# Optimization experiments

Measured on AMD Instinct MI355X. Metric: run time of the kernel, lower is better.

## Reference

```python
import jax, jax.numpy as jnp
import numpy as np

B, L, D = 2, 2048, 1536
H = 12            # num_heads == num_key_value_heads
FDIM = 16         # feature_dim (per-head q/k dim)
HD = D // H       # head_dim = 128 (per-head v dim)
EPS = 1e-12
W_STD = 0.02


def setup_inputs() -> dict:
    key = jax.random.key(0)
    k0, k1, k2, k3, k4 = jax.random.split(key, 5)
    hidden_states = jax.random.normal(k0, (B, L, D), dtype=jnp.float32)
    Wq = jax.random.normal(k1, (D, H * FDIM), dtype=jnp.float32) * W_STD
    Wk = jax.random.normal(k2, (D, H * FDIM), dtype=jnp.float32) * W_STD
    Wv = jax.random.normal(k3, (D, H * HD), dtype=jnp.float32) * W_STD
    Wo = jax.random.normal(k4, (H * HD, D), dtype=jnp.float32) * W_STD
    return {"hidden_states": hidden_states, "Wq": Wq, "Wk": Wk, "Wv": Wv, "Wo": Wo}


def _split_heads(x, h):
    b, l, hd = x.shape
    return x.reshape(b, l, h, hd // h).transpose(0, 2, 1, 3)  # b h l d


def reference(hidden_states, Wq, Wk, Wv, Wo):
    b, l, _ = hidden_states.shape
    q = _split_heads(hidden_states @ Wq, H)  # [b,h,l,FDIM]
    k = _split_heads(hidden_states @ Wk, H)  # [b,h,l,FDIM]
    v = _split_heads(hidden_states @ Wv, H)  # [b,h,l,HD]

    # parallel_based(q, k, v, eps, use_scale=True, use_normalize=True)
    q = q * (FDIM ** -0.5)
    s = jnp.einsum('bhld,bhmd->bhlm', q, k)            # raw qk scores
    attn = 1.0 + s + 0.5 * s * s                        # 2nd-order Taylor of exp
    causal = jnp.tril(jnp.ones((l, l), dtype=bool))
    attn = jnp.where(causal, attn, 0.0)
    o = jnp.einsum('bhlm,bhmd->bhld', attn, v)          # [b,h,l,HD]
    z = attn.sum(axis=-1)                               # causal normalizer [b,h,l]
    o = o / (z[..., None] + EPS)

    o = o.transpose(0, 2, 1, 3).reshape(b, l, H * HD)   # b l (h d)
    return o @ Wo
```

## Files before the change

kernel.cpp:

```cpp
#include <hip/hip_runtime.h>
#include <hip/hip_bf16.h>

typedef short short8 __attribute__((ext_vector_type(8)));
typedef float f32x4  __attribute__((ext_vector_type(4)));
typedef float f32x16 __attribute__((ext_vector_type(16)));
typedef unsigned int u32x4 __attribute__((ext_vector_type(4)));

union V16   { u32x4 v; short8 s; };
union U16x8 { u32x4 v; unsigned short u[8]; };
union FB4   { u32x4 v; float f[4]; };
union BF2U  { __hip_bfloat162 h; unsigned int u; };

__device__ inline unsigned short f2bf(float f) {
  union { float f; unsigned int u; } x; x.f = f;
  unsigned int u = x.u + 0x7fffu + ((x.u >> 16) & 1u);
  return (unsigned short)(u >> 16);
}

__device__ __forceinline__ unsigned int pkbf(float a, float b) {
  BF2U p; p.h = __float22bfloat162_rn(make_float2(a, b)); return p.u;
}

__device__ __forceinline__ void plswap(unsigned int& a, unsigned int& b) {
  asm("v_permlane32_swap_b32 %0, %1" : "+v"(a), "+v"(b));
}

__device__ __forceinline__ int probe_fp32(const unsigned short* hs) {
  int bad = 0;
#pragma unroll
  for (int i = 0; i < 64; ++i) {
    unsigned int e = (hs[2 * i] >> 7) & 0xFFu;
    if (e >= 0xFEu || (e > 0u && e < 0x60u)) bad++;
  }
  return bad >= 6;
}

__device__ __forceinline__ void gl_lds16(const unsigned short* g, unsigned short* l) {
  __builtin_amdgcn_global_load_lds(
      (const __attribute__((address_space(1))) unsigned int*)g,
      (__attribute__((address_space(3))) unsigned int*)l, 16, 0, 0);
}

__global__ __launch_bounds__(256) void w_tr(const void* __restrict__ Wq,
                                            const void* __restrict__ Wk,
                                            const void* __restrict__ Wv,
                                            const void* __restrict__ Wo,
                                            const void* __restrict__ hs,
                                            unsigned short* __restrict__ WT,
                                            unsigned short* __restrict__ WoT,
                                            unsigned short* __restrict__ hsb) {
  __shared__ unsigned short t[32][33];
  __shared__ int sf;
  if (threadIdx.x == 0) sf = probe_fp32((const unsigned short*)hs);
  __syncthreads();
  const int f = sf;
  const int z = blockIdx.z;
  if (z == 4) {
    size_t i0 = ((size_t)(blockIdx.y * 48 + blockIdx.x) * 256 + threadIdx.x) * 8;
    if (f) {
      const float* in = (const float*)hs;
      FB4 a, b; a.v = *(const u32x4*)&in[i0]; b.v = *(const u32x4*)&in[i0 + 4];
      U16x8 p;
#pragma unroll
      for (int j = 0; j < 4; ++j) { p.u[j] = f2bf(a.f[j]); p.u[j + 4] = f2bf(b.f[j]); }
      *(u32x4*)&hsb[i0] = p.v;
    } else {
      *(u32x4*)&hsb[i0] = *(const u32x4*)((const unsigned short*)hs + i0);
    }
    return;
  }
  if (blockIdx.y >= 48) return;
  const void* in_; unsigned short* out; int C;
  if      (z == 0) { in_ = Wq; out = WT;              C = 192;  }
  else if (z == 1) { in_ = Wk; out = WT + 192 * 1536; C = 192;  }
  else if (z == 2) { in_ = Wv; out = WT + 384 * 1536; C = 1536; }
  else             { in_ = Wo; out = WoT;             C = 1536; }
  const int c0 = blockIdx.x * 32;
  if (c0 >= C) return;
  const int tx = threadIdx.x & 31, ty = threadIdx.x >> 5;
  const int r0 = blockIdx.y * 32;
#pragma unroll
  for (int i = 0; i < 4; ++i) {
    size_t idx = (size_t)(r0 + ty + 8 * i) * C + (c0 + tx);
    t[ty + 8 * i][tx] = f ? f2bf(((const float*)in_)[idx])
                          : ((const unsigned short*)in_)[idx];
  }
  __syncthreads();
#pragma unroll
  for (int i = 0; i < 4; ++i)
    out[(size_t)(c0 + ty + 8 * i) * 1536 + (r0 + tx)] = t[tx][ty + 8 * i];
}

__global__ __launch_bounds__(256) void tr_v(const unsigned short* __restrict__ in_,
                                            unsigned short* __restrict__ out,
                                            int R, int C, int ldin,
                                            long long in_bstride, long long out_bstride) {
  __shared__ unsigned short t[32][33];
  const size_t ibase = (size_t)blockIdx.z * in_bstride;
  const size_t obase = (size_t)blockIdx.z * out_bstride;
  const int tx = threadIdx.x & 31, ty = threadIdx.x >> 5;
  const int r0 = blockIdx.y * 32, c0 = blockIdx.x * 32;
#pragma unroll
  for (int i = 0; i < 4; ++i)
    t[ty + 8 * i][tx] = in_[ibase + (size_t)(r0 + ty + 8 * i) * ldin + (c0 + tx)];
  __syncthreads();
#pragma unroll
  for (int i = 0; i < 4; ++i)
    out[obase + (size_t)(c0 + ty + 8 * i) * R + (r0 + tx)] = t[tx][ty + 8 * i];
}

__global__ __launch_bounds__(256) void gemm_bt(const unsigned short* __restrict__ A,
                                               const unsigned short* __restrict__ BT,
                                               void* __restrict__ C_,
                                               int M, int N, int K,
                                               const unsigned short* __restrict__ probe_src) {
  __shared__ unsigned short As[2][128][64];
  __shared__ unsigned short Bs[2][128][64];
  const int m0 = blockIdx.y * 128, n0 = blockIdx.x * 128;
  const int tid = threadIdx.x;
  const int lane = tid & 63, w = tid >> 6;
  const int wr = w >> 1, wc = w & 1;
  const int quad = lane >> 4, mrow = lane & 15;

  const int sr = lane >> 3;
  const int sc = ((lane & 7) ^ (lane >> 3)) * 8;
  const int fsw = (mrow & 7);

  const f32x4 zf = {0.f, 0.f, 0.f, 0.f};
  f32x4 acc[4][4];
#pragma unroll
  for (int mt = 0; mt < 4; ++mt)
#pragma unroll
    for (int nt = 0; nt < 4; ++nt) acc[mt][nt] = zf;

  const int nk = K >> 6;
#pragma unroll
  for (int j = 0; j < 4; ++j) {
    const int r = 32 * w + 8 * j + sr;
    gl_lds16(&A [(size_t)(m0 + r) * K + sc], &As[0][32 * w + 8 * j][0]);
    gl_lds16(&BT[(size_t)(n0 + r) * K + sc], &Bs[0][32 * w + 8 * j][0]);
  }

  for (int ks = 0; ks < nk; ++ks) {
    const int cur = ks & 1;
    __syncthreads();
    if (ks + 1 < nk) {
      const int k1 = (ks + 1) << 6;
#pragma unroll
      for (int j = 0; j < 4; ++j) {
        const int r = 32 * w + 8 * j + sr;
        gl_lds16(&A [(size_t)(m0 + r) * K + k1 + sc], &As[cur ^ 1][32 * w + 8 * j][0]);
        gl_lds16(&BT[(size_t)(n0 + r) * K + k1 + sc], &Bs[cur ^ 1][32 * w + 8 * j][0]);
      }
    }
#pragma unroll
    for (int kq = 0; kq < 2; ++kq) {
      short8 afr[4], bfr[4];
#pragma unroll
      for (int mt = 0; mt < 4; ++mt) {
        V16 u; u.v = *(const u32x4*)&As[cur][wr * 64 + mt * 16 + mrow][((kq * 4 + quad) ^ fsw) * 8];
        afr[mt] = u.s;
      }
#pragma unroll
      for (int nt = 0; nt < 4; ++nt) {
        V16 u; u.v = *(const u32x4*)&Bs[cur][wc * 64 + nt * 16 + mrow][((kq * 4 + quad) ^ fsw) * 8];
        bfr[nt] = u.s;
      }
#pragma unroll
      for (int mt = 0; mt < 4; ++mt)
#pragma unroll
        for (int nt = 0; nt < 4; ++nt)
          acc[mt][nt] = __builtin_amdgcn_mfma_f32_16x16x32_bf16(afr[mt], bfr[nt], acc[mt][nt], 0, 0, 0);
    }
  }

  const int of = probe_src ? probe_fp32(probe_src) : 0;
#pragma unroll
  for (int mt = 0; mt < 4; ++mt)
#pragma unroll
    for (int nt = 0; nt < 4; ++nt)
#pragma unroll
      for (int r = 0; r < 4; ++r) {
        int grow = m0 + wr * 64 + mt * 16 + quad * 4 + r;
        int gcol = n0 + wc * 64 + nt * 16 + mrow;
        size_t idx = (size_t)grow * N + gcol;
        if (of) ((float*)C_)[idx] = acc[mt][nt][r];
        else    ((unsigned short*)C_)[idx] = f2bf(acc[mt][nt][r]);
      }
}

__global__ __launch_bounds__(256, 3) void attn_based(const unsigned short* __restrict__ qkv,
                                                     const unsigned short* __restrict__ vT,
                                                     unsigned short* __restrict__ obuf) {
  __shared__ unsigned short Vs[2][128][64];
  __shared__ float zbuf[2][32];
  const int LD = 1920;
  const int bh = blockIdx.x;
  const int qt = 31 - blockIdx.y;
  const int b = bh / 12, h = bh % 12;
  const int tid = threadIdx.x;
  const int lane = tid & 63, w = tid >> 6;
  const int qsub = w & 1, kvp = w >> 1;
  const int col = lane & 31, hi = lane >> 5;

  const int q0 = qt * 64 + qsub * 32;
  const int q_abs = q0 + col;

  V16 bq; bq.v = *(const u32x4*)&qkv[(size_t)(b * 2048 + q_abs) * LD + h * 16 + hi * 8];

  const unsigned short* kptr =
      &qkv[(size_t)(b * 2048 + kvp * 32 + col) * LD + 192 + h * 16 + hi * 8];

  const unsigned short* vbase = vT + (size_t)(bh * 128) * 2048;

  const f32x16 z16 = {0.f,0.f,0.f,0.f,0.f,0.f,0.f,0.f,0.f,0.f,0.f,0.f,0.f,0.f,0.f,0.f};
  f32x16 oacc[4];
#pragma unroll
  for (int nc = 0; nc < 4; ++nc) oacc[nc] = z16;
  float zcA[4] = {0.f, 0.f, 0.f, 0.f};

#define STAGE_V(KV0, BUF)                                                     \
  {                                                                           \
    _Pragma("unroll")                                                         \
    for (int j = 0; j < 4; ++j) {                                             \
      const int row = 32 * w + 8 * j + (lane >> 3);                           \
      gl_lds16(vbase + (size_t)row * 2048 + (KV0) + ((lane & 7) ^ (lane >> 3)) * 8, \
               &Vs[BUF][32 * w + 8 * j][0]);                                  \
    }                                                                         \
  }

  STAGE_V(0, 0);
  V16 kf; kf.v = *(const u32x4*)kptr;
  __syncthreads();

  for (int t = 0; t <= qt; ++t) {
    const int cur = t & 1;
    if (t < qt) STAGE_V((t + 1) * 64, cur ^ 1);

    V16 kfn;
    kptr += (size_t)64 * LD;
    if (t < qt) kfn.v = *(const u32x4*)kptr;

    const bool live = (t < qt) | (kvp <= qsub);
    if (live) {
      f32x16 st = __builtin_amdgcn_mfma_f32_32x32x16_bf16(kf.s, bq.s, z16, 0, 0, 0);
      const int kv0 = t * 64 + kvp * 32;
      const bool diag = (t == qt) & (kvp == qsub);
      float pr[16];
      if (diag) {
#pragma unroll
        for (int r = 0; r < 16; ++r) {
          float s = st[r];
          float a = fmaf(s, fmaf(s, 0.03125f, 0.25f), 1.0f);
          const int kvr = kv0 + (r & 3) + 8 * (r >> 2) + 4 * hi;
          a = (kvr <= q_abs) ? a : 0.0f;
          zcA[r & 3] += a; pr[r] = a;
        }
      } else {
#pragma unroll
        for (int r = 0; r < 16; ++r) {
          float s = st[r];
          float a = fmaf(s, fmaf(s, 0.03125f, 0.25f), 1.0f);
          zcA[r & 3] += a; pr[r] = a;
        }
      }

      union PA { short8 s; unsigned int wd[4]; } pa0, pa1;
      {
        unsigned int x0 = pkbf(pr[0], pr[1]), x1 = pkbf(pr[2], pr[3]);
        unsigned int y0 = pkbf(pr[4], pr[5]), y1 = pkbf(pr[6], pr[7]);
        plswap(x0, y0); plswap(x1, y1);
        pa0.wd[0] = x0; pa0.wd[1] = x1; pa0.wd[2] = y0; pa0.wd[3] = y1;
      }
      {
        unsigned int x0 = pkbf(pr[8], pr[9]),  x1 = pkbf(pr[10], pr[11]);
        unsigned int y0 = pkbf(pr[12], pr[13]), y1 = pkbf(pr[14], pr[15]);
        plswap(x0, y0); plswap(x1, y1);
        pa1.wd[0] = x0; pa1.wd[1] = x1; pa1.wd[2] = y0; pa1.wd[3] = y1;
      }

      __builtin_amdgcn_s_setprio(1);
#pragma unroll
      for (int nc = 0; nc < 4; ++nc) {
        const int hd = nc * 32 + col;
        V16 v0, v1;
        v0.v = *(const u32x4*)&Vs[cur][hd][(((kvp * 4 + hi)     ^ (hd & 7)) * 8)];
        v1.v = *(const u32x4*)&Vs[cur][hd][(((kvp * 4 + 2 + hi) ^ (hd & 7)) * 8)];
        oacc[nc] = __builtin_amdgcn_mfma_f32_32x32x16_bf16(pa0.s, v0.s, oacc[nc], 0, 0, 0);
        oacc[nc] = __builtin_amdgcn_mfma_f32_32x32x16_bf16(pa1.s, v1.s, oacc[nc], 0, 0, 0);
      }
      __builtin_amdgcn_s_setprio(0);
    }
    __syncthreads();
    if (t < qt) kf = kfn;
  }

  float zcol = (zcA[0] + zcA[1]) + (zcA[2] + zcA[3]);
  zcol += __shfl_xor(zcol, 32, 64);

  float* fbuf = (float*)&Vs[0][0][0];
  if (w >= 2) {
    const int base = (w & 1) * 4096;
#pragma unroll
    for (int nc = 0; nc < 4; ++nc)
#pragma unroll
      for (int g = 0; g < 4; ++g) {
        f32x4 v = {oacc[nc][4 * g], oacc[nc][4 * g + 1],
                   oacc[nc][4 * g + 2], oacc[nc][4 * g + 3]};
        *(f32x4*)&fbuf[base + ((nc * 4 + g) * 64 + lane) * 4] = v;
      }
    if (lane < 32) zbuf[w & 1][lane] = zcol;
  }
  __syncthreads();
  if (w < 2) {
    const int base = w * 4096;
#pragma unroll
    for (int nc = 0; nc < 4; ++nc)
#pragma unroll
      for (int g = 0; g < 4; ++g) {
        f32x4 v = *(const f32x4*)&fbuf[base + ((nc * 4 + g) * 64 + lane) * 4];
#pragma unroll
        for (int r = 0; r < 4; ++r) oacc[nc][4 * g + r] += v[r];
      }
    const float zinv = 1.0f / (zcol + zbuf[w][col] + 1e-12f);
#pragma unroll
    for (int g = 0; g < 4; ++g)
#pragma unroll
      for (int rr = 0; rr < 4; ++rr) {
        const int qrow = rr + 8 * g + 4 * hi;
        const float iv = __shfl(zinv, qrow, 64);
        const size_t base_o = (size_t)(b * 2048 + q0 + qrow) * 1536 + h * 128 + col;
#pragma unroll
        for (int nc = 0; nc < 4; ++nc)
          obuf[base_o + nc * 32] = f2bf(oacc[nc][4 * g + rr] * iv);
      }
  }
#undef STAGE_V
}

extern "C" void kernel_launch(void* const* d_in, const int* in_sizes, int n_in,
                              void* d_out, int out_size, void* d_ws, size_t ws_size,
                              hipStream_t stream) {
  const void* hs = d_in[0];
  const void* Wq = d_in[1];
  const void* Wk = d_in[2];
  const void* Wv = d_in[3];
  const void* Wo = d_in[4];
  const unsigned short* hsp = (const unsigned short*)hs;

  unsigned short* ws   = (unsigned short*)d_ws;
  unsigned short* WT   = ws;
  unsigned short* WoT  = WT + 1920 * 1536;
  unsigned short* qkvb = WoT + 1536 * 1536;
  unsigned short* hsb  = qkvb + 4096 * 1920;
  unsigned short* vT   = hsb + 4096 * 1536;
  unsigned short* obuf = hsb;

  w_tr<<<dim3(48, 64, 5), 256, 0, stream>>>(Wq, Wk, Wv, Wo, hs, WT, WoT, hsb);

  gemm_bt<<<dim3(15, 32, 1), 256, 0, stream>>>(hsb, WT, qkvb, 4096, 1920, 1536, nullptr);

  tr_v<<<dim3(48, 64, 2), 256, 0, stream>>>(qkvb + 384, vT, 2048, 1536, 1920,
                                            (long long)2048 * 1920, (long long)1536 * 2048);

  attn_based<<<dim3(24, 32, 1), 256, 0, stream>>>(qkvb, vT, obuf);

  gemm_bt<<<dim3(12, 32, 1), 256, 0, stream>>>(obuf, WoT, d_out, 4096, 1536, 1536, hsp);
}
```

Measured before the change: 223.2 us.

## Replace GEMM with 8-wave 256x128 tile, triple-buffered, interleaved MFMA schedule

Swaps the 4-wave 128x128 double-buffered GEMM for an 8-wave kernel with 256x128 tiles and a three-stage LDS ring. Global-to-LDS loads are issued two steps ahead and split across four compute phases. Barriers, sched_barrier pins and setprio bracket each group of MFMAs so the waves stay in lockstep and load issue overlaps matrix math. The aim is to hide global load latency and LDS read stalls in both projection GEMMs. The cost is more LDS per block, more barriers and hand-tuned vmcnt waits that are fragile.

```diff
diff --git a/kernel.cpp b/kernel.cpp
--- a/kernel.cpp
+++ b/kernel.cpp
@@ -40,6 +40,8 @@
       (const __attribute__((address_space(1))) unsigned int*)g,
       (__attribute__((address_space(3))) unsigned int*)l, 16, 0, 0);
 }
+
+#define PIN() __builtin_amdgcn_sched_barrier(0)
 
 __global__ __launch_bounds__(256) void w_tr(const void* __restrict__ Wq,
                                             const void* __restrict__ Wk,
@@ -109,22 +111,31 @@
     out[obase + (size_t)(c0 + ty + 8 * i) * R + (r0 + tx)] = t[tx][ty + 8 * i];
 }
 
-__global__ __launch_bounds__(256) void gemm_bt(const unsigned short* __restrict__ A,
-                                               const unsigned short* __restrict__ BT,
-                                               void* __restrict__ C_,
-                                               int M, int N, int K,
-                                               const unsigned short* __restrict__ probe_src) {
-  __shared__ unsigned short As[2][128][64];
-  __shared__ unsigned short Bs[2][128][64];
-  const int m0 = blockIdx.y * 128, n0 = blockIdx.x * 128;
+__global__ __launch_bounds__(512, 2) void gemm8(const unsigned short* __restrict__ A,
+                                                const unsigned short* __restrict__ BT,
+                                                void* __restrict__ C_,
+                                                int M, int N, int K,
+                                                const unsigned short* __restrict__ probe_src) {
+  __shared__ unsigned short As[3][256][64];
+  __shared__ unsigned short Bs[3][128][64];
+  const int m0 = blockIdx.y * 256, n0 = blockIdx.x * 128;
   const int tid = threadIdx.x;
   const int lane = tid & 63, w = tid >> 6;
   const int wr = w >> 1, wc = w & 1;
   const int quad = lane >> 4, mrow = lane & 15;
+  const int fsw = (mrow & 7);
 
   const int sr = lane >> 3;
-  const int sc = ((lane & 7) ^ (lane >> 3)) * 8;
-  const int fsw = (mrow & 7);
+  const int sc = ((lane & 7) ^ sr) * 8;
+  const unsigned short* Ab = A  + (size_t)(m0 + 32 * w + sr) * K + sc;
+  const unsigned short* Bb = BT + (size_t)(n0 + 16 * w + sr) * K + sc;
+
+#define STAGE_A(T2, J) gl_lds16(Ab + (size_t)(8 * (J)) * K + (size_t)(T2) * 64, \
+                                &As[(T2) % 3][32 * w + 8 * (J)][0])
+#define STAGE_B(T2, J) gl_lds16(Bb + (size_t)(8 * (J)) * K + (size_t)(T2) * 64, \
+                                &Bs[(T2) % 3][16 * w + 8 * (J)][0])
+#define RD_A(dst, mt, kq) { V16 u_; u_.v = *(const u32x4*)&As[cur][wr * 64 + (mt) * 16 + mrow][(((kq) * 4 + quad) ^ fsw) * 8]; dst = u_.s; }
+#define RD_B(dst, nt, kq) { V16 u_; u_.v = *(const u32x4*)&Bs[cur][wc * 64 + (nt) * 16 + mrow][(((kq) * 4 + quad) ^ fsw) * 8]; dst = u_.s; }
 
   const f32x4 zf = {0.f, 0.f, 0.f, 0.f};
   f32x4 acc[4][4];
@@ -134,44 +145,88 @@
     for (int nt = 0; nt < 4; ++nt) acc[mt][nt] = zf;
 
   const int nk = K >> 6;
-#pragma unroll
-  for (int j = 0; j < 4; ++j) {
-    const int r = 32 * w + 8 * j + sr;
-    gl_lds16(&A [(size_t)(m0 + r) * K + sc], &As[0][32 * w + 8 * j][0]);
-    gl_lds16(&BT[(size_t)(n0 + r) * K + sc], &Bs[0][32 * w + 8 * j][0]);
-  }
-
-  for (int ks = 0; ks < nk; ++ks) {
-    const int cur = ks & 1;
-    __syncthreads();
-    if (ks + 1 < nk) {
-      const int k1 = (ks + 1) << 6;
-#pragma unroll
-      for (int j = 0; j < 4; ++j) {
-        const int r = 32 * w + 8 * j + sr;
-        gl_lds16(&A [(size_t)(m0 + r) * K + k1 + sc], &As[cur ^ 1][32 * w + 8 * j][0]);
-        gl_lds16(&BT[(size_t)(n0 + r) * K + k1 + sc], &Bs[cur ^ 1][32 * w + 8 * j][0]);
-      }
-    }
-#pragma unroll
-    for (int kq = 0; kq < 2; ++kq) {
-      short8 afr[4], bfr[4];
-#pragma unroll
-      for (int mt = 0; mt < 4; ++mt) {
-        V16 u; u.v = *(const u32x4*)&As[cur][wr * 64 + mt * 16 + mrow][((kq * 4 + quad) ^ fsw) * 8];
-        afr[mt] = u.s;
-      }
-#pragma unroll
-      for (int nt = 0; nt < 4; ++nt) {
-        V16 u; u.v = *(const u32x4*)&Bs[cur][wc * 64 + nt * 16 + mrow][((kq * 4 + quad) ^ fsw) * 8];
-        bfr[nt] = u.s;
-      }
-#pragma unroll
-      for (int mt = 0; mt < 4; ++mt)
-#pragma unroll
-        for (int nt = 0; nt < 4; ++nt)
-          acc[mt][nt] = __builtin_amdgcn_mfma_f32_16x16x32_bf16(afr[mt], bfr[nt], acc[mt][nt], 0, 0, 0);
-    }
+
+#pragma unroll
+  for (int j = 0; j < 4; ++j) STAGE_A(0, j);
+#pragma unroll
+  for (int j = 0; j < 2; ++j) STAGE_B(0, j);
+#pragma unroll
+  for (int j = 0; j < 4; ++j) STAGE_A(1, j);
+#pragma unroll
+  for (int j = 0; j < 2; ++j) STAGE_B(1, j);
+  asm volatile("s_waitcnt vmcnt(6)" ::: "memory");
+  PIN();
+  __builtin_amdgcn_s_barrier();
+  PIN();
+
+  for (int t = 0; t < nk; ++t) {
+    const int cur = t % 3;
+    const int t2 = t + 2;
+    const bool st = t2 < nk;
+    short8 a0, a1, a2, a3, b0, b1, b2, b3;
+
+    RD_A(a0, 0, 0); RD_A(a1, 1, 0);
+    RD_B(b0, 0, 0); RD_B(b1, 1, 0); RD_B(b2, 2, 0); RD_B(b3, 3, 0);
+    if (st) { STAGE_A(t2, 0); STAGE_A(t2, 1); }
+    PIN(); __builtin_amdgcn_s_barrier(); PIN();
+    __builtin_amdgcn_s_setprio(1);
+    acc[0][0] = __builtin_amdgcn_mfma_f32_16x16x32_bf16(a0, b0, acc[0][0], 0, 0, 0);
+    acc[0][1] = __builtin_amdgcn_mfma_f32_16x16x32_bf16(a0, b1, acc[0][1], 0, 0, 0);
+    acc[0][2] = __builtin_amdgcn_mfma_f32_16x16x32_bf16(a0, b2, acc[0][2], 0, 0, 0);
+    acc[0][3] = __builtin_amdgcn_mfma_f32_16x16x32_bf16(a0, b3, acc[0][3], 0, 0, 0);
+    acc[1][0] = __builtin_amdgcn_mfma_f32_16x16x32_bf16(a1, b0, acc[1][0], 0, 0, 0);
+    acc[1][1] = __builtin_amdgcn_mfma_f32_16x16x32_bf16(a1, b1, acc[1][1], 0, 0, 0);
+    acc[1][2] = __builtin_amdgcn_mfma_f32_16x16x32_bf16(a1, b2, acc[1][2], 0, 0, 0);
+    acc[1][3] = __builtin_amdgcn_mfma_f32_16x16x32_bf16(a1, b3, acc[1][3], 0, 0, 0);
+    __builtin_amdgcn_s_setprio(0);
+    PIN(); __builtin_amdgcn_s_barrier(); PIN();
+
+    RD_A(a2, 2, 0); RD_A(a3, 3, 0);
+    if (st) { STAGE_A(t2, 2); STAGE_A(t2, 3); }
+    PIN(); __builtin_amdgcn_s_barrier(); PIN();
+    __builtin_amdgcn_s_setprio(1);
+    acc[2][0] = __builtin_amdgcn_mfma_f32_16x16x32_bf16(a2, b0, acc[2][0], 0, 0, 0);
+    acc[2][1] = __builtin_amdgcn_mfma_f32_16x16x32_bf16(a2, b1, acc[2][1], 0, 0, 0);
+    acc[2][2] = __builtin_amdgcn_mfma_f32_16x16x32_bf16(a2, b2, acc[2][2], 0, 0, 0);
+    acc[2][3] = __builtin_amdgcn_mfma_f32_16x16x32_bf16(a2, b3, acc[2][3], 0, 0, 0);
+    acc[3][0] = __builtin_amdgcn_mfma_f32_16x16x32_bf16(a3, b0, acc[3][0], 0, 0, 0);
+    acc[3][1] = __builtin_amdgcn_mfma_f32_16x16x32_bf16(a3, b1, acc[3][1], 0, 0, 0);
+    acc[3][2] = __builtin_amdgcn_mfma_f32_16x16x32_bf16(a3, b2, acc[3][2], 0, 0, 0);
+    acc[3][3] = __builtin_amdgcn_mfma_f32_16x16x32_bf16(a3, b3, acc[3][3], 0, 0, 0);
+    __builtin_amdgcn_s_setprio(0);
+    PIN(); __builtin_amdgcn_s_barrier(); PIN();
+
+    RD_A(a0, 0, 1); RD_A(a1, 1, 1);
+    RD_B(b0, 0, 1); RD_B(b1, 1, 1); RD_B(b2, 2, 1); RD_B(b3, 3, 1);
+    if (st) { STAGE_B(t2, 0); STAGE_B(t2, 1); }
+    PIN(); __builtin_amdgcn_s_barrier(); PIN();
+    __builtin_amdgcn_s_setprio(1);
+    acc[0][0] = __builtin_amdgcn_mfma_f32_16x16x32_bf16(a0, b0, acc[0][0], 0, 0, 0);
+    acc[0][1] = __builtin_amdgcn_mfma_f32_16x16x32_bf16(a0, b1, acc[0][1], 0, 0, 0);
+    acc[0][2] = __builtin_amdgcn_mfma_f32_16x16x32_bf16(a0, b2, acc[0][2], 0, 0, 0);
+    acc[0][3] = __builtin_amdgcn_mfma_f32_16x16x32_bf16(a0, b3, acc[0][3], 0, 0, 0);
+    acc[1][0] = __builtin_amdgcn_mfma_f32_16x16x32_bf16(a1, b0, acc[1][0], 0, 0, 0);
+    acc[1][1] = __builtin_amdgcn_mfma_f32_16x16x32_bf16(a1, b1, acc[1][1], 0, 0, 0);
+    acc[1][2] = __builtin_amdgcn_mfma_f32_16x16x32_bf16(a1, b2, acc[1][2], 0, 0, 0);
+    acc[1][3] = __builtin_amdgcn_mfma_f32_16x16x32_bf16(a1, b3, acc[1][3], 0, 0, 0);
+    __builtin_amdgcn_s_setprio(0);
+    PIN(); __builtin_amdgcn_s_barrier(); PIN();
+
+    RD_A(a2, 2, 1); RD_A(a3, 3, 1);
+    PIN(); __builtin_amdgcn_s_barrier(); PIN();
+    __builtin_amdgcn_s_setprio(1);
+    acc[2][0] = __builtin_amdgcn_mfma_f32_16x16x32_bf16(a2, b0, acc[2][0], 0, 0, 0);
+    acc[2][1] = __builtin_amdgcn_mfma_f32_16x16x32_bf16(a2, b1, acc[2][1], 0, 0, 0);
+    acc[2][2] = __builtin_amdgcn_mfma_f32_16x16x32_bf16(a2, b2, acc[2][2], 0, 0, 0);
+    acc[2][3] = __builtin_amdgcn_mfma_f32_16x16x32_bf16(a2, b3, acc[2][3], 0, 0, 0);
+    acc[3][0] = __builtin_amdgcn_mfma_f32_16x16x32_bf16(a3, b0, acc[3][0], 0, 0, 0);
+    acc[3][1] = __builtin_amdgcn_mfma_f32_16x16x32_bf16(a3, b1, acc[3][1], 0, 0, 0);
+    acc[3][2] = __builtin_amdgcn_mfma_f32_16x16x32_bf16(a3, b2, acc[3][2], 0, 0, 0);
+    acc[3][3] = __builtin_amdgcn_mfma_f32_16x16x32_bf16(a3, b3, acc[3][3], 0, 0, 0);
+    __builtin_amdgcn_s_setprio(0);
+    if (st) asm volatile("s_waitcnt vmcnt(6)" ::: "memory");
+    else    asm volatile("s_waitcnt vmcnt(0)" ::: "memory");
+    PIN(); __builtin_amdgcn_s_barrier(); PIN();
   }
 
   const int of = probe_src ? probe_fp32(probe_src) : 0;
@@ -187,6 +242,10 @@
         if (of) ((float*)C_)[idx] = acc[mt][nt][r];
         else    ((unsigned short*)C_)[idx] = f2bf(acc[mt][nt][r]);
       }
+#undef STAGE_A
+#undef STAGE_B
+#undef RD_A
+#undef RD_B
 }
 
 __global__ __launch_bounds__(256, 3) void attn_based(const unsigned short* __restrict__ qkv,
@@ -358,12 +417,12 @@
 
   w_tr<<<dim3(48, 64, 5), 256, 0, stream>>>(Wq, Wk, Wv, Wo, hs, WT, WoT, hsb);
 
-  gemm_bt<<<dim3(15, 32, 1), 256, 0, stream>>>(hsb, WT, qkvb, 4096, 1920, 1536, nullptr);
+  gemm8<<<dim3(15, 16, 1), 512, 0, stream>>>(hsb, WT, qkvb, 4096, 1920, 1536, nullptr);
 
   tr_v<<<dim3(48, 64, 2), 256, 0, stream>>>(qkvb + 384, vT, 2048, 1536, 1920,
                                             (long long)2048 * 1920, (long long)1536 * 2048);
 
   attn_based<<<dim3(24, 32, 1), 256, 0, stream>>>(qkvb, vT, obuf);
 
-  gemm_bt<<<dim3(12, 32, 1), 256, 0, stream>>>(obuf, WoT, d_out, 4096, 1536, 1536, hsp);
-}
+  gemm8<<<dim3(12, 16, 1), 512, 0, stream>>>(obuf, WoT, d_out, 4096, 1536, 1536, hsp);
+}
```

New measurement: 239.7 us. 7.3% more time.

## Fuse V transpose into QKV GEMM epilogue via LDS staging

Applied to the files above, without the earlier changes.

Removes the separate tr_v kernel. The QKV projection GEMM now writes the V columns directly in transposed [b,h,d,l] layout, staging each wave's tile through shared memory and issuing 16-byte row stores. Only Q/K go to a narrower 384-wide buffer, and the attention kernel's leading dimension is updated to match. This saves a launch plus a full read and write of V, but adds an LDS round trip in the GEMM epilogue.

```diff
diff --git a/kernel.cpp b/kernel.cpp
--- a/kernel.cpp
+++ b/kernel.cpp
@@ -91,31 +91,15 @@
     out[(size_t)(c0 + ty + 8 * i) * 1536 + (r0 + tx)] = t[tx][ty + 8 * i];
 }
 
-__global__ __launch_bounds__(256) void tr_v(const unsigned short* __restrict__ in_,
-                                            unsigned short* __restrict__ out,
-                                            int R, int C, int ldin,
-                                            long long in_bstride, long long out_bstride) {
-  __shared__ unsigned short t[32][33];
-  const size_t ibase = (size_t)blockIdx.z * in_bstride;
-  const size_t obase = (size_t)blockIdx.z * out_bstride;
-  const int tx = threadIdx.x & 31, ty = threadIdx.x >> 5;
-  const int r0 = blockIdx.y * 32, c0 = blockIdx.x * 32;
-#pragma unroll
-  for (int i = 0; i < 4; ++i)
-    t[ty + 8 * i][tx] = in_[ibase + (size_t)(r0 + ty + 8 * i) * ldin + (c0 + tx)];
-  __syncthreads();
-#pragma unroll
-  for (int i = 0; i < 4; ++i)
-    out[obase + (size_t)(c0 + ty + 8 * i) * R + (r0 + tx)] = t[tx][ty + 8 * i];
-}
-
 __global__ __launch_bounds__(256) void gemm_bt(const unsigned short* __restrict__ A,
                                                const unsigned short* __restrict__ BT,
                                                void* __restrict__ C_,
-                                               int M, int N, int K,
+                                               int M, int NB, int K, int ldC,
+                                               unsigned short* __restrict__ vTout,
                                                const unsigned short* __restrict__ probe_src) {
-  __shared__ unsigned short As[2][128][64];
-  __shared__ unsigned short Bs[2][128][64];
+  __shared__ unsigned short smem[4 * 128 * 64];
+#define AS(buf, r, c) smem[(((buf) * 128) + (r)) * 64 + (c)]
+#define BS(buf, r, c) smem[(((2 + (buf)) * 128) + (r)) * 64 + (c)]
   const int m0 = blockIdx.y * 128, n0 = blockIdx.x * 128;
   const int tid = threadIdx.x;
   const int lane = tid & 63, w = tid >> 6;
@@ -137,8 +121,8 @@
 #pragma unroll
   for (int j = 0; j < 4; ++j) {
     const int r = 32 * w + 8 * j + sr;
-    gl_lds16(&A [(size_t)(m0 + r) * K + sc], &As[0][32 * w + 8 * j][0]);
-    gl_lds16(&BT[(size_t)(n0 + r) * K + sc], &Bs[0][32 * w + 8 * j][0]);
+    gl_lds16(&A [(size_t)(m0 + r) * K + sc], &AS(0, 32 * w + 8 * j, 0));
+    gl_lds16(&BT[(size_t)(n0 + r) * K + sc], &BS(0, 32 * w + 8 * j, 0));
   }
 
   for (int ks = 0; ks < nk; ++ks) {
@@ -149,8 +133,8 @@
 #pragma unroll
       for (int j = 0; j < 4; ++j) {
         const int r = 32 * w + 8 * j + sr;
-        gl_lds16(&A [(size_t)(m0 + r) * K + k1 + sc], &As[cur ^ 1][32 * w + 8 * j][0]);
-        gl_lds16(&BT[(size_t)(n0 + r) * K + k1 + sc], &Bs[cur ^ 1][32 * w + 8 * j][0]);
+        gl_lds16(&A [(size_t)(m0 + r) * K + k1 + sc], &AS(cur ^ 1, 32 * w + 8 * j, 0));
+        gl_lds16(&BT[(size_t)(n0 + r) * K + k1 + sc], &BS(cur ^ 1, 32 * w + 8 * j, 0));
       }
     }
 #pragma unroll
@@ -158,12 +142,12 @@
       short8 afr[4], bfr[4];
 #pragma unroll
       for (int mt = 0; mt < 4; ++mt) {
-        V16 u; u.v = *(const u32x4*)&As[cur][wr * 64 + mt * 16 + mrow][((kq * 4 + quad) ^ fsw) * 8];
+        V16 u; u.v = *(const u32x4*)&AS(cur, wr * 64 + mt * 16 + mrow, ((kq * 4 + quad) ^ fsw) * 8);
         afr[mt] = u.s;
       }
 #pragma unroll
       for (int nt = 0; nt < 4; ++nt) {
-        V16 u; u.v = *(const u32x4*)&Bs[cur][wc * 64 + nt * 16 + mrow][((kq * 4 + quad) ^ fsw) * 8];
+        V16 u; u.v = *(const u32x4*)&BS(cur, wc * 64 + nt * 16 + mrow, ((kq * 4 + quad) ^ fsw) * 8);
         bfr[nt] = u.s;
       }
 #pragma unroll
@@ -174,19 +158,45 @@
     }
   }
 
-  const int of = probe_src ? probe_fp32(probe_src) : 0;
-#pragma unroll
-  for (int mt = 0; mt < 4; ++mt)
-#pragma unroll
-    for (int nt = 0; nt < 4; ++nt)
-#pragma unroll
-      for (int r = 0; r < 4; ++r) {
-        int grow = m0 + wr * 64 + mt * 16 + quad * 4 + r;
-        int gcol = n0 + wc * 64 + nt * 16 + mrow;
-        size_t idx = (size_t)grow * N + gcol;
-        if (of) ((float*)C_)[idx] = acc[mt][nt][r];
-        else    ((unsigned short*)C_)[idx] = f2bf(acc[mt][nt][r]);
-      }
+  __syncthreads();
+  if (vTout != nullptr && n0 >= 384) {
+    unsigned short* T = smem + w * (64 * 72);
+#pragma unroll
+    for (int mt = 0; mt < 4; ++mt)
+#pragma unroll
+      for (int nt = 0; nt < 4; ++nt)
+#pragma unroll
+        for (int r = 0; r < 4; ++r)
+          T[(nt * 16 + mrow) * 72 + mt * 16 + quad * 4 + r] = f2bf(acc[mt][nt][r]);
+    asm volatile("s_waitcnt lgkmcnt(0)" ::: "memory");
+    const int h  = (n0 - 384) >> 7;
+    const int gb = (m0 + wr * 64) >> 11;
+    const int l0 = (m0 + wr * 64) & 2047;
+    const size_t vrow0 = ((size_t)(gb * 12 + h) << 7) + wc * 64;
+#pragma unroll
+    for (int i = 0; i < 8; ++i) {
+      const int row = (lane >> 3) + 8 * i;
+      const int ch  = (lane & 7) * 8;
+      u32x4 vv = *(const u32x4*)&T[row * 72 + ch];
+      *(u32x4*)&vTout[(vrow0 + row) * 2048 + l0 + ch] = vv;
+    }
+  } else {
+    const int of = probe_src ? probe_fp32(probe_src) : 0;
+#pragma unroll
+    for (int mt = 0; mt < 4; ++mt)
+#pragma unroll
+      for (int nt = 0; nt < 4; ++nt)
+#pragma unroll
+        for (int r = 0; r < 4; ++r) {
+          int grow = m0 + wr * 64 + mt * 16 + quad * 4 + r;
+          int gcol = n0 + wc * 64 + nt * 16 + mrow;
+          size_t idx = (size_t)grow * ldC + gcol;
+          if (of) ((float*)C_)[idx] = acc[mt][nt][r];
+          else    ((unsigned short*)C_)[idx] = f2bf(acc[mt][nt][r]);
+        }
+  }
+#undef AS
+#undef BS
 }
 
 __global__ __launch_bounds__(256, 3) void attn_based(const unsigned short* __restrict__ qkv,
@@ -194,7 +204,7 @@
                                                      unsigned short* __restrict__ obuf) {
   __shared__ unsigned short Vs[2][128][64];
   __shared__ float zbuf[2][32];
-  const int LD = 1920;
+  const int LD = 384;
   const int bh = blockIdx.x;
   const int qt = 31 - blockIdx.y;
   const int b = bh / 12, h = bh % 12;
@@ -352,18 +362,17 @@
   unsigned short* WT   = ws;
   unsigned short* WoT  = WT + 1920 * 1536;
   unsigned short* qkvb = WoT + 1536 * 1536;
-  unsigned short* hsb  = qkvb + 4096 * 1920;
+  unsigned short* hsb  = qkvb + 4096 * 384;
   unsigned short* vT   = hsb + 4096 * 1536;
   unsigned short* obuf = hsb;
 
   w_tr<<<dim3(48, 64, 5), 256, 0, stream>>>(Wq, Wk, Wv, Wo, hs, WT, WoT, hsb);
 
-  gemm_bt<<<dim3(15, 32, 1), 256, 0, stream>>>(hsb, WT, qkvb, 4096, 1920, 1536, nullptr);
-
-  tr_v<<<dim3(48, 64, 2), 256, 0, stream>>>(qkvb + 384, vT, 2048, 1536, 1920,
-                                            (long long)2048 * 1920, (long long)1536 * 2048);
+  gemm_bt<<<dim3(15, 32, 1), 256, 0, stream>>>(hsb, WT, qkvb, 4096, 1920, 1536,
+                                               384, vT, nullptr);
 
   attn_based<<<dim3(24, 32, 1), 256, 0, stream>>>(qkvb, vT, obuf);
 
-  gemm_bt<<<dim3(12, 32, 1), 256, 0, stream>>>(obuf, WoT, d_out, 4096, 1536, 1536, hsp);
-}
+  gemm_bt<<<dim3(12, 32, 1), 256, 0, stream>>>(obuf, WoT, d_out, 4096, 1536, 1536,
+                                               1536, nullptr, hsp);
+}
```

Result: faster. 207.1 us (-7.2%).
